# Kernel optimization log

Measured on AMD Instinct MI355X. Metric: run time of the kernel, lower is better.

The kernel has to match this reference:

```python
import jax, jax.numpy as jnp
import numpy as np

HDR_H, HDR_W = 16, 32  # HDR_map_shape[:2]


def _light_dirs_and_coeff():
    # Matl: unit direction per HDR texel, matching the torch double loop.
    phi = (jnp.arange(HDR_H, dtype=jnp.float32) / HDR_H) * jnp.pi          # (16,)
    theta = (jnp.arange(HDR_W, dtype=jnp.float32) / HDR_W) * (2 * jnp.pi)  # (32,)
    sp, cp = jnp.sin(phi)[:, None], jnp.cos(phi)[:, None]                  # (16,1)
    st, ct = jnp.sin(theta)[None, :], jnp.cos(theta)[None, :]              # (1,32)
    dirs = jnp.stack([st * sp, jnp.broadcast_to(cp, (HDR_H, HDR_W)), -ct * sp], axis=-1)  # (16,32,3)
    dirs = dirs / jnp.linalg.norm(dirs, axis=-1, keepdims=True)
    Matl = dirs.reshape(-1, 3).T                                            # (3, M=512)
    coeff = jnp.broadcast_to(sp[:, :, None], (HDR_H, 1, 3))                 # (16,1,3), sin(phi) per row
    return Matl, coeff


def setup_inputs() -> dict:
    key = jax.random.key(0)
    k1, k2, k3 = jax.random.split(key, 3)
    B, H, W = 2, 512, 512
    env = jax.random.uniform(k1, (B, HDR_H, HDR_W, 3), dtype=jnp.float32)
    normal = jax.random.uniform(k2, (B, H, W, 3), dtype=jnp.float32)
    albedo = jax.random.uniform(k3, (B, 3, H, W), dtype=jnp.float32)
    return {"env": env, "normal": normal, "albedo": albedo}


def reference(env, normal, albedo):
    B, H, W, _ = normal.shape
    Matl, coeff = _light_dirs_and_coeff()
    # HDR weighting: env * sin(phi) row coefficient -> (B, M, 3)
    hdr = (env * coeff[None]).reshape(B, HDR_H * HDR_W, 3)
    # Normal map: flip channel order (::-1) then decode to [-1,1]
    n = (normal[..., ::-1] - 0.5) * 2.0
    Matn = n.reshape(B, H * W, 3)                                           # (B, N, 3)
    # relu-clamped dot products against all light directions: (B, N, M)
    Matd = jax.nn.relu(jnp.einsum('bnk,km->bnm', Matn, Matl))
    # weight by HDR and reduce over light directions (same math as the per-channel torch loop)
    light = jnp.einsum('bnm,bmc->bnc', Matd, hdr)                           # (B, N, 3)
    lightmap = light.reshape(B, H, W, 3).transpose(0, 3, 1, 2)              # (B, 3, H, W)
    diffuse = (lightmap / 50.0) * albedo
    return diffuse
```

## Files before the change

kernel.cpp:

```cpp
#include <hip/hip_runtime.h>
#include <hip/hip_bf16.h>


constexpr int HW     = 512 * 512;
constexpr int WAVES  = 4;
constexpr int GROUPS = 8;

typedef _Float16 half2v __attribute__((ext_vector_type(2)));
typedef _Float16 half8  __attribute__((ext_vector_type(8)));
typedef float    f32x4  __attribute__((ext_vector_type(4)));

__device__ constexpr float SPc[8] = {
    0.195090322f, 0.382683432f, 0.555570233f, 0.707106781f,
    0.831469612f, 0.923879533f, 0.980785280f, 1.0f };
__device__ constexpr float CPc[8] = {
    0.980785280f, 0.923879533f, 0.831469612f, 0.707106781f,
    0.555570233f, 0.382683432f, 0.195090322f, 0.0f };
__device__ constexpr float STc[32] = {
    0.0f,          0.195090322f,  0.382683432f,  0.555570233f,
    0.707106781f,  0.831469612f,  0.923879533f,  0.980785280f,
    1.0f,          0.980785280f,  0.923879533f,  0.831469612f,
    0.707106781f,  0.555570233f,  0.382683432f,  0.195090322f,
    0.0f,         -0.195090322f, -0.382683432f, -0.555570233f,
   -0.707106781f, -0.831469612f, -0.923879533f, -0.980785280f,
   -1.0f,         -0.980785280f, -0.923879533f, -0.831469612f,
   -0.707106781f, -0.555570233f, -0.382683432f, -0.195090322f };
__device__ constexpr float CTc[32] = {
    1.0f,          0.980785280f,  0.923879533f,  0.831469612f,
    0.707106781f,  0.555570233f,  0.382683432f,  0.195090322f,
    0.0f,         -0.195090322f, -0.382683432f, -0.555570233f,
   -0.707106781f, -0.831469612f, -0.923879533f, -0.980785280f,
   -1.0f,         -0.980785280f, -0.923879533f, -0.831469612f,
   -0.707106781f, -0.555570233f, -0.382683432f, -0.195090322f,
    0.0f,          0.195090322f,  0.382683432f,  0.555570233f,
    0.707106781f,  0.831469612f,  0.923879533f,  0.980785280f };

union h8u { unsigned u[4]; half8 v; half2v h2[4]; };

__global__ __launch_bounds__(256, 4)
void env_render_fused(const float* __restrict__ env,
                      const float* __restrict__ normal,
                      const float* __restrict__ albedo,
                      float* __restrict__ out)
{
    __shared__ float lds_env[16 * 32 * 3];
    __shared__ half8 lds_hf[512];
    __shared__ float Wred[WAVES][9];

    const int b    = blockIdx.y;
    const int t    = threadIdx.x;
    const int lane = t & 63, wave = t >> 6;
    const int ch   = lane & 15, cg = lane >> 4;

    #pragma unroll
    for (int q = 0; q < 6; ++q)
        lds_env[t + q * 256] = env[(size_t)b * 1536 + t + q * 256];
    __syncthreads();

    #pragma unroll
    for (int ss = 0; ss < 2; ++ss) {
        const int s = t + ss * 256;
        const int tile = s >> 6, ln = s & 63;
        const int kc = ln >> 4, chh = ln & 15;
        const int j  = tile * 4 + kc;
        half8 f;
        #pragma unroll
        for (int e = 0; e < 8; ++e) {
            const int i = e + 1;
            float v = 0.f;
            if (chh < 3 && !(i == 8 && j >= 16)) {
                const int i2 = 16 - i, j2 = (j + 16) & 31;
                v = (lds_env[(i * 32 + j) * 3 + chh] +
                     lds_env[(i2 * 32 + j2) * 3 + chh]) * (SPc[e] * 0.01f);
            }
            f[e] = (_Float16)v;
        }
        lds_hf[s] = f;
    }

    float W[9];
    #pragma unroll
    for (int q = 0; q < 9; ++q) W[q] = 0.0f;
    if (t < 240) {
        int i, j;
        if (t < 224) { i = 1 + (t >> 5); j = t & 31; }
        else         { i = 8;            j = t - 224; }
        const int i2 = 16 - i, j2 = (j + 16) & 31;
        const float sp = SPc[i - 1], cp = CPc[i - 1];
        const float st = STc[j],     ct = CTc[j];
        const float dx = st * sp, dy = cp, dz = -ct * sp;
        const float scale = sp * 0.01f;
        const float* ea = lds_env + (i * 32 + j) * 3;
        const float* eb = lds_env + (i2 * 32 + j2) * 3;
        const float hd0 = (ea[0] - eb[0]) * scale;
        const float hd1 = (ea[1] - eb[1]) * scale;
        const float hd2 = (ea[2] - eb[2]) * scale;
        W[0] = dx * hd0; W[1] = dx * hd1; W[2] = dx * hd2;
        W[3] = dy * hd0; W[4] = dy * hd1; W[5] = dy * hd2;
        W[6] = dz * hd0; W[7] = dz * hd1; W[8] = dz * hd2;
    }
    #pragma unroll
    for (int q = 0; q < 9; ++q) {
        float v = W[q];
        #pragma unroll
        for (int off = 32; off > 0; off >>= 1) v += __shfl_down(v, off);
        if (lane == 0) Wred[wave][q] = v;
    }
    __syncthreads();

    float Wl[9];
    #pragma unroll
    for (int q = 0; q < 9; ++q)
        Wl[q] = Wred[0][q] + Wred[1][q] + Wred[2][q] + Wred[3][q];

    half8 Hf[8];
    #pragma unroll
    for (int tl = 0; tl < 8; ++tl) Hf[tl] = lds_hf[tl * 64 + lane];

    half2v st2[4], ct2[4], sp2[4], cp2[4];
    #pragma unroll
    for (int p = 0; p < 4; ++p) {
        st2[p] = half2v{(_Float16)STc[(2 * p) * 4 + cg], (_Float16)STc[(2 * p + 1) * 4 + cg]};
        ct2[p] = half2v{(_Float16)CTc[(2 * p) * 4 + cg], (_Float16)CTc[(2 * p + 1) * 4 + cg]};
        sp2[p] = half2v{(_Float16)SPc[2 * p], (_Float16)SPc[2 * p + 1]};
        cp2[p] = half2v{(_Float16)CPc[2 * p], (_Float16)CPc[2 * p + 1]};
    }

    const int g0 = (blockIdx.x * WAVES + wave) * GROUPS;
    float nr[GROUPS][3];
    #pragma unroll
    for (int g = 0; g < GROUPS; ++g) {
        const int pix = (g0 + g) * 16 + ch;
        const float* p = normal + ((size_t)b * HW + pix) * 3;
        nr[g][0] = p[0]; nr[g][1] = p[1]; nr[g][2] = p[2];
    }

    #pragma unroll
    for (int g = 0; g < GROUPS; ++g) {
        const int pix = (g0 + g) * 16 + ch;
        const size_t base = (size_t)b * 3 * HW + pix;
        const float al0 = albedo[base];
        const float al1 = albedo[base + HW];
        const float al2 = albedo[base + 2 * HW];

        const float nx = fmaf(nr[g][2], 2.0f, -1.0f);
        const float ny = fmaf(nr[g][1], 2.0f, -1.0f);
        const float nz = fmaf(nr[g][0], 2.0f, -1.0f);

        const _Float16 nxh = (_Float16)nx, nyh = (_Float16)ny, nzh = (_Float16)nz;
        const half2v nx2 = {nxh, nxh}, ny2 = {nyh, nyh}, nz2 = {nzh, nzh};

        half2v u2[4], nyc2[4];
        #pragma unroll
        for (int p = 0; p < 4; ++p) {
            u2[p]   = nx2 * st2[p] - nz2 * ct2[p];
            nyc2[p] = ny2 * cp2[p];
        }

        f32x4 acc = {0.f, 0.f, 0.f, 0.f};
        #pragma unroll
        for (int tl = 0; tl < 8; ++tl) {
            const _Float16 uh = (tl & 1) ? u2[tl >> 1].y : u2[tl >> 1].x;
            const half2v ub = {uh, uh};
            h8u pk;
            #pragma unroll
            for (int p = 0; p < 4; ++p) {
                const half2v d2 = sp2[p] * ub + nyc2[p];
                pk.h2[p] = d2;
                pk.u[p] &= 0x7FFF7FFFu;
            }
            acc = __builtin_amdgcn_mfma_f32_16x16x32_f16(Hf[tl], pk.v, acc, 0, 0, 0);
        }

        if (cg == 0) {
            const float l0 = acc[0] + fmaf(nx, Wl[0], fmaf(ny, Wl[3], nz * Wl[6]));
            const float l1 = acc[1] + fmaf(nx, Wl[1], fmaf(ny, Wl[4], nz * Wl[7]));
            const float l2 = acc[2] + fmaf(nx, Wl[2], fmaf(ny, Wl[5], nz * Wl[8]));
            out[base]          = l0 * al0;
            out[base + HW]     = l1 * al1;
            out[base + 2 * HW] = l2 * al2;
        }
    }
}

extern "C" void kernel_launch(void* const* d_in, const int* in_sizes, int n_in,
                              void* d_out, int out_size, void* d_ws, size_t ws_size,
                              hipStream_t stream)
{
    const float* env    = (const float*)d_in[0];
    const float* normal = (const float*)d_in[1];
    const float* albedo = (const float*)d_in[2];
    float* out          = (float*)d_out;

    const int B = in_sizes[0] / (16 * 32 * 3);

    dim3 grid((HW / 16) / (WAVES * GROUPS), B);
    env_render_fused<<<grid, 256, 0, stream>>>(env, normal, albedo, out);
}
```

Measured before the change: 19.15 us.

## Stage normals and lighting through LDS for coalesced vector global I/O

Each wave now loads its contiguous block of normals into shared memory with 16-byte vector loads, instead of each lane issuing strided scalar loads. Per-pixel lighting is written to shared memory, and a final pass multiplies by albedo using vector loads and stores. Before, only a quarter of the lanes did scattered output writes. Pixels per wave are doubled (GROUPS 8→16), which halves the grid. The cosine table is replaced by shifted or derived sine values. This adds shared-memory footprint (about 24KB more per block) and an extra barrier.

```diff
diff --git a/kernel.cpp b/kernel.cpp
--- a/kernel.cpp
+++ b/kernel.cpp
@@ -1,10 +1,9 @@
 #include <hip/hip_runtime.h>
-#include <hip/hip_bf16.h>
 
 
 constexpr int HW     = 512 * 512;
 constexpr int WAVES  = 4;
-constexpr int GROUPS = 8;
+constexpr int GROUPS = 16;
 
 typedef _Float16 half2v __attribute__((ext_vector_type(2)));
 typedef _Float16 half8  __attribute__((ext_vector_type(8)));
@@ -33,7 +32,7 @@
    -1.0f,         -0.980785280f, -0.923879533f, -0.831469612f,
    -0.707106781f, -0.555570233f, -0.382683432f, -0.195090322f,
     0.0f,          0.195090322f,  0.382683432f,  0.555570233f,
-    0.707106781f,  0.831469612f,  0.923879533f,  0.980785280f };
+    0.707106781f,  0.923879533f,  0.923879533f,  0.980785280f };
 
 union h8u { unsigned u[4]; half8 v; half2v h2[4]; };
 
@@ -45,6 +44,8 @@
 {
     __shared__ float lds_env[16 * 32 * 3];
     __shared__ half8 lds_hf[512];
+    __shared__ float lds_nrm[WAVES][768];
+    __shared__ float lds_light[WAVES][768];
     __shared__ float Wred[WAVES][9];
 
     const int b    = blockIdx.y;
@@ -52,9 +53,20 @@
     const int lane = t & 63, wave = t >> 6;
     const int ch   = lane & 15, cg = lane >> 4;
 
+    const int wavepx0 = (blockIdx.x * WAVES + wave) * (GROUPS * 16);
+
     #pragma unroll
     for (int q = 0; q < 6; ++q)
         lds_env[t + q * 256] = env[(size_t)b * 1536 + t + q * 256];
+
+    {
+        const float* nsrc = normal + ((size_t)b * HW + wavepx0) * 3;
+        #pragma unroll
+        for (int q = 0; q < 3; ++q) {
+            const f32x4 v = *(const f32x4*)(nsrc + q * 256 + lane * 4);
+            *(f32x4*)&lds_nrm[wave][q * 256 + lane * 4] = v;
+        }
+    }
     __syncthreads();
 
     #pragma unroll
@@ -87,7 +99,11 @@
         else         { i = 8;            j = t - 224; }
         const int i2 = 16 - i, j2 = (j + 16) & 31;
         const float sp = SPc[i - 1], cp = CPc[i - 1];
-        const float st = STc[j],     ct = CTc[j];
+        const int jm = j & 15;
+        const float sbase = (jm == 0) ? 0.0f : ((jm <= 8) ? SPc[jm - 1] : CPc[jm - 9]);
+        const float cbase = (jm == 0) ? 1.0f : ((jm <= 8) ? CPc[jm - 1] : -SPc[jm - 9]);
+        const float st = (j < 16) ? sbase : -sbase;
+        const float ct = (j < 16) ? cbase : -cbase;
         const float dx = st * sp, dy = cp, dz = -ct * sp;
         const float scale = sp * 0.01f;
         const float* ea = lds_env + (i * 32 + j) * 3;
@@ -120,32 +136,26 @@
     half2v st2[4], ct2[4], sp2[4], cp2[4];
     #pragma unroll
     for (int p = 0; p < 4; ++p) {
-        st2[p] = half2v{(_Float16)STc[(2 * p) * 4 + cg], (_Float16)STc[(2 * p + 1) * 4 + cg]};
-        ct2[p] = half2v{(_Float16)CTc[(2 * p) * 4 + cg], (_Float16)CTc[(2 * p + 1) * 4 + cg]};
+        const int ja = (2 * p) * 4 + cg, jb = (2 * p + 1) * 4 + cg;
+        st2[p] = half2v{(_Float16)STc[ja], (_Float16)STc[jb]};
+        const float cta = ((ja + 8) & 31) < 16 ?  STc[(ja + 8) & 31] : STc[(ja + 8) & 31];
+        const float ctb = ((jb + 8) & 31) < 16 ?  STc[(jb + 8) & 31] : STc[(jb + 8) & 31];
+        ct2[p] = half2v{(_Float16)STc[(ja + 8) & 31], (_Float16)STc[(jb + 8) & 31]};
+        (void)cta; (void)ctb;
         sp2[p] = half2v{(_Float16)SPc[2 * p], (_Float16)SPc[2 * p + 1]};
         cp2[p] = half2v{(_Float16)CPc[2 * p], (_Float16)CPc[2 * p + 1]};
     }
 
-    const int g0 = (blockIdx.x * WAVES + wave) * GROUPS;
-    float nr[GROUPS][3];
     #pragma unroll
     for (int g = 0; g < GROUPS; ++g) {
-        const int pix = (g0 + g) * 16 + ch;
-        const float* p = normal + ((size_t)b * HW + pix) * 3;
-        nr[g][0] = p[0]; nr[g][1] = p[1]; nr[g][2] = p[2];
-    }
-
-    #pragma unroll
-    for (int g = 0; g < GROUPS; ++g) {
-        const int pix = (g0 + g) * 16 + ch;
-        const size_t base = (size_t)b * 3 * HW + pix;
-        const float al0 = albedo[base];
-        const float al1 = albedo[base + HW];
-        const float al2 = albedo[base + 2 * HW];
-
-        const float nx = fmaf(nr[g][2], 2.0f, -1.0f);
-        const float ny = fmaf(nr[g][1], 2.0f, -1.0f);
-        const float nz = fmaf(nr[g][0], 2.0f, -1.0f);
+        const int pxl = g * 16 + ch;
+        const float n0 = lds_nrm[wave][pxl * 3 + 0];
+        const float n1 = lds_nrm[wave][pxl * 3 + 1];
+        const float n2 = lds_nrm[wave][pxl * 3 + 2];
+
+        const float nx = fmaf(n2, 2.0f, -1.0f);
+        const float ny = fmaf(n1, 2.0f, -1.0f);
+        const float nz = fmaf(n0, 2.0f, -1.0f);
 
         const _Float16 nxh = (_Float16)nx, nyh = (_Float16)ny, nzh = (_Float16)nz;
         const half2v nx2 = {nxh, nxh}, ny2 = {nyh, nyh}, nz2 = {nzh, nzh};
@@ -173,13 +183,22 @@
         }
 
         if (cg == 0) {
-            const float l0 = acc[0] + fmaf(nx, Wl[0], fmaf(ny, Wl[3], nz * Wl[6]));
-            const float l1 = acc[1] + fmaf(nx, Wl[1], fmaf(ny, Wl[4], nz * Wl[7]));
-            const float l2 = acc[2] + fmaf(nx, Wl[2], fmaf(ny, Wl[5], nz * Wl[8]));
-            out[base]          = l0 * al0;
-            out[base + HW]     = l1 * al1;
-            out[base + 2 * HW] = l2 * al2;
-        }
+            lds_light[wave][pxl]       = acc[0] + fmaf(nx, Wl[0], fmaf(ny, Wl[3], nz * Wl[6]));
+            lds_light[wave][256 + pxl] = acc[1] + fmaf(nx, Wl[1], fmaf(ny, Wl[4], nz * Wl[7]));
+            lds_light[wave][512 + pxl] = acc[2] + fmaf(nx, Wl[2], fmaf(ny, Wl[5], nz * Wl[8]));
+        }
+    }
+    __syncthreads();
+
+    const size_t bbase = (size_t)b * 3 * HW + wavepx0;
+    #pragma unroll
+    for (int c = 0; c < 3; ++c) {
+        const f32x4 av = *(const f32x4*)(albedo + bbase + (size_t)c * HW + lane * 4);
+        const f32x4 lv = *(const f32x4*)&lds_light[wave][c * 256 + lane * 4];
+        f32x4 ov;
+        #pragma unroll
+        for (int k = 0; k < 4; ++k) ov[k] = av[k] * lv[k];
+        *(f32x4*)(out + bbase + (size_t)c * HW + lane * 4) = ov;
     }
 }
 
```

After: 18.72 us. 1.02x faster.
